# Kernel tuning notes

Hardware: AMD Instinct MI355X
Metric: run time of the kernel (lower is better)

Reference implementation:

```python
import jax, jax.numpy as jnp
import numpy as np
from jax import lax

B, S, F_IN, H = 64, 512, 128, 512

def setup_inputs() -> dict:
    key = jax.random.key(0)
    ks = jax.random.split(key, 7)
    s = 1.0 / np.sqrt(H)
    return {
        "inputs": jax.random.normal(ks[0], (B, S, F_IN), dtype=jnp.float32),
        "W_ih": jax.random.normal(ks[1], (4 * H, F_IN), dtype=jnp.float32) * s,
        "W_hh": jax.random.normal(ks[2], (4 * H, H), dtype=jnp.float32) * s,
        "b_ih": jax.random.normal(ks[3], (4 * H,), dtype=jnp.float32) * s,
        "b_hh": jax.random.normal(ks[4], (4 * H,), dtype=jnp.float32) * s,
        "W_out": jax.random.normal(ks[5], (F_IN, H), dtype=jnp.float32) * s,
        "b_out": jax.random.normal(ks[6], (F_IN,), dtype=jnp.float32) * s,
    }

def reference(inputs, W_ih, W_hh, b_ih, b_hh, W_out, b_out):
    # inputs: [B, S, F]. Inference path: y=None, future=0 -> scan over all S steps.
    b, seq, _ = inputs.shape
    h = W_hh.shape[1]
    # Precompute input-to-gate projections for all timesteps: [S, B, 4H]
    x_gates = jnp.einsum("bsf,gf->sbg", inputs, W_ih) + b_ih + b_hh

    def step(carry, xg):
        h_t, c_t = carry
        gates = xg + h_t @ W_hh.T  # [B, 4H]
        i_g, f_g, g_g, o_g = jnp.split(gates, 4, axis=-1)
        i_g = jax.nn.sigmoid(i_g)
        f_g = jax.nn.sigmoid(f_g)
        g_g = jnp.tanh(g_g)
        o_g = jax.nn.sigmoid(o_g)
        c_t = f_g * c_t + i_g * g_g
        h_t = o_g * jnp.tanh(c_t)
        out = h_t @ W_out.T + b_out  # [B, F]
        return (h_t, c_t), out

    h0 = jnp.zeros((b, h), dtype=inputs.dtype)
    c0 = jnp.zeros((b, h), dtype=inputs.dtype)
    _, outs = lax.scan(step, (h0, c0), x_gates)  # outs: [S, B, F]
    return jnp.transpose(outs, (1, 0, 2))  # [B, S, F]
```

## Files before the change

kernel.cpp:

```cpp
#include <hip/hip_runtime.h>

typedef float f32x4 __attribute__((ext_vector_type(4)));

namespace {
constexpr int Bn = 64, Sn = 512, Fn = 128, Hn = 512;
constexpr int NWG = 256, NTHR = 512;
constexpr int HXS = 644;
constexpr int PQS = 581;
constexpr int RING0 = 1024;
}

__device__ __forceinline__ float sigmoid_f(float v) {
    return 1.0f / (1.0f + __expf(-v));
}
__device__ __forceinline__ float tanh_f(float v) {
    v = fminf(fmaxf(v, -15.0f), 15.0f);
    const float e = __expf(-2.0f * v);
    return (1.0f - e) / (1.0f + e);
}

__global__ __launch_bounds__(NTHR, 2)
void lstm_persist(const float* __restrict__ x,
                  const float* __restrict__ Wih,
                  const float* __restrict__ Whh,
                  const float* __restrict__ bih,
                  const float* __restrict__ bhh,
                  const float* __restrict__ Wout,
                  const float* __restrict__ bout,
                  float* __restrict__ out,
                  float* __restrict__ ws)
{
    const int w = blockIdx.x, t = threadIdx.x;
    const int bw = w & 7, rw = w >> 3;

    const int q  = t & 31;
    const int r4 = t >> 5;
    const int k0 = 20 * q;

    const int out_fi  = (t >> 1) & 3;
    const int out_bb  = (t >> 3) & 7;
    const int out_ksl = ((t >> 6) << 1) | (t & 1);

    __shared__ float hx[8][HXS];
    __shared__ float part[32 * PQS];
    __shared__ float opart[4][8][9];
    __shared__ float gb[64];
    __shared__ float cst[16][9];
    __shared__ float bo[4];

    f32x4 wreg[4][5];
#pragma unroll
    for (int i = 0; i < 4; ++i) {
        const int r = 4 * r4 + i;
        const int G = (r >> 4) * Hn + rw * 16 + (r & 15);
#pragma unroll
        for (int j = 0; j < 5; ++j) {
            const int kk = k0 + 4 * j;
            if (kk < Hn) wreg[i][j] = *(const f32x4*)(Whh + (size_t)G * Hn + kk);
            else         wreg[i][j] = *(const f32x4*)(Wih + (size_t)G * Fn + (kk - Hn));
        }
    }

    if (t < 64) {
        const int G = (t >> 4) * Hn + rw * 16 + (t & 15);
        gb[t] = bih[G] + bhh[G];
    }
    if (t < 4) bo[t] = bout[rw * 4 + t];
    if (t < 128) cst[t >> 3][t & 7] = 0.0f;

    unsigned* const bar = (unsigned*)ws;
    float* const ring = ws + RING0;

    if (t < 128) {
        const int ul = t & 15, bb = (t >> 4) & 7;
        float* hdst = ring + (size_t)(Bn * Hn) +
                      (size_t)(8 * bw + bb) * Hn + (16 * rw + ul);
        const float z = 0.0f;
        asm volatile("global_store_dword %0, %1, off sc0 sc1"
                     :: "v"(hdst), "v"(z) : "memory");
    }
    asm volatile("s_waitcnt vmcnt(0)" ::: "memory");
    __syncthreads();
    if (t == 0) {
        unsigned* gcnt = bar + 32 * ((w >> 4) + 1);
        const unsigned old = atomicAdd(gcnt, 1u);
        if (old == 15u) atomicAdd(bar, 1u);
        int guard = 0;
        while (__hip_atomic_load(bar, __ATOMIC_RELAXED,
                                 __HIP_MEMORY_SCOPE_AGENT) < 16u) {
            __builtin_amdgcn_s_sleep(1);
            if (++guard > 100000) break;
        }
    }
    __syncthreads();

    for (int k = 0; k <= Sn; ++k) {
        const int slot = (k & 1) ^ 1;
        const float* hsrc = ring + (size_t)slot * (Bn * Hn) + (size_t)bw * 8 * Hn;
        f32x4 v0, v1;
        {
            const float* p0 = hsrc + 4 * t;
            const float* p1 = p0 + 2048;
            asm volatile(
                "global_load_dwordx4 %0, %2, off sc0 sc1\n\t"
                "global_load_dwordx4 %1, %3, off sc0 sc1\n\t"
                "s_waitcnt vmcnt(0)"
                : "=&v"(v0), "=&v"(v1)
                : "v"(p0), "v"(p1));
        }
        {
            int fi = t;
            *(f32x4*)&hx[fi >> 7][(fi & 127) * 4] = v0;
            fi = t + 512;
            *(f32x4*)&hx[fi >> 7][(fi & 127) * 4] = v1;
        }
        if (k < Sn && t < 256) {
            const int bb = t >> 5, f4 = (t & 31) * 4;
            const f32x4 v = *(const f32x4*)(x + (size_t)(8 * bw + bb) * Sn * Fn +
                                            (size_t)k * Fn + f4);
            *(f32x4*)&hx[bb][Hn + f4] = v;
        }
        __syncthreads();

        if (k < Sn) {
            float acc[4][8];
#pragma unroll
            for (int i = 0; i < 4; ++i)
#pragma unroll
                for (int ib = 0; ib < 8; ++ib) acc[i][ib] = 0.0f;
#pragma unroll
            for (int j = 0; j < 5; ++j) {
                f32x4 hv[4];
#pragma unroll
                for (int ib = 0; ib < 4; ++ib)
                    hv[ib] = *(const f32x4*)&hx[ib][k0 + 4 * j];
#pragma unroll
                for (int i = 0; i < 4; ++i)
#pragma unroll
                    for (int ib = 0; ib < 4; ++ib)
                        acc[i][ib] += wreg[i][j].x * hv[ib].x + wreg[i][j].y * hv[ib].y +
                                      wreg[i][j].z * hv[ib].z + wreg[i][j].w * hv[ib].w;
#pragma unroll
                for (int ib = 0; ib < 4; ++ib)
                    hv[ib] = *(const f32x4*)&hx[4 + ib][k0 + 4 * j];
#pragma unroll
                for (int i = 0; i < 4; ++i)
#pragma unroll
                    for (int ib = 0; ib < 4; ++ib)
                        acc[i][4 + ib] += wreg[i][j].x * hv[ib].x + wreg[i][j].y * hv[ib].y +
                                          wreg[i][j].z * hv[ib].z + wreg[i][j].w * hv[ib].w;
            }
#pragma unroll
            for (int i = 0; i < 4; ++i)
#pragma unroll
                for (int ib = 0; ib < 8; ++ib)
                    part[q * PQS + (4 * r4 + i) * 9 + ib] = acc[i][ib];
        }

        if (k >= 1 && t < 256) {
            const float* wo = Wout + (size_t)(rw * 4 + out_fi) * Hn + out_ksl * 64;
            const float* hrow = &hx[out_bb][out_ksl * 64];
            float oa = 0.0f;
#pragma unroll
            for (int jj = 0; jj < 16; ++jj) {
                const f32x4 wv = *(const f32x4*)(wo + 4 * jj);
                const f32x4 hv = *(const f32x4*)(hrow + 4 * jj);
                oa += wv.x * hv.x + wv.y * hv.y + wv.z * hv.z + wv.w * hv.w;
            }
            opart[out_fi][out_bb][out_ksl] = oa;
        }
        __syncthreads();

        if (k < Sn && t < 128) {
            const int ul = t & 15, bb = (t >> 4) & 7;
            float g4[4];
#pragma unroll
            for (int gate = 0; gate < 4; ++gate) {
                const int r = gate * 16 + ul;
                float s = gb[r];
#pragma unroll
                for (int qq = 0; qq < 32; ++qq) s += part[qq * PQS + r * 9 + bb];
                g4[gate] = s;
            }
            const float ig = sigmoid_f(g4[0]);
            const float fg = sigmoid_f(g4[1]);
            const float gg = tanh_f(g4[2]);
            const float og = sigmoid_f(g4[3]);
            const float cn = fg * cst[ul][bb] + ig * gg;
            cst[ul][bb] = cn;
            const float hn = og * tanh_f(cn);
            float* hdst = ring + (size_t)(k & 1) * (Bn * Hn) +
                          (size_t)(8 * bw + bb) * Hn + (16 * rw + ul);
            asm volatile("global_store_dword %0, %1, off sc0 sc1"
                         :: "v"(hdst), "v"(hn) : "memory");
        } else if (k >= 1 && t >= 128 && t < 160) {
            const int fi = (t - 128) >> 3, bb = (t - 128) & 7;
            float s = bo[fi];
#pragma unroll
            for (int qq = 0; qq < 8; ++qq) s += opart[fi][bb][qq];
            out[(size_t)(8 * bw + bb) * Sn * Fn + (size_t)(k - 1) * Fn + rw * 4 + fi] = s;
        }

        if (k < Sn) {
            asm volatile("s_waitcnt vmcnt(0)" ::: "memory");
            __syncthreads();
            if (t == 0) {
                const unsigned gen = (unsigned)(k + 2);
                unsigned* gcnt = bar + 32 * ((w >> 4) + 1);
                const unsigned old = atomicAdd(gcnt, 1u);
                if (old == 16u * gen - 1u) atomicAdd(bar, 1u);
                const unsigned target = 16u * gen;
                int guard = 0;
                while (__hip_atomic_load(bar, __ATOMIC_RELAXED,
                                         __HIP_MEMORY_SCOPE_AGENT) < target) {
                    __builtin_amdgcn_s_sleep(1);
                    if (++guard > 100000) break;
                }
            }
            __syncthreads();
        }
    }
}

extern "C" void kernel_launch(void* const* d_in, const int* in_sizes, int n_in,
                              void* d_out, int out_size, void* d_ws, size_t ws_size,
                              hipStream_t stream) {
    (void)in_sizes; (void)n_in; (void)out_size; (void)ws_size;
    const float* x    = (const float*)d_in[0];
    const float* Wih  = (const float*)d_in[1];
    const float* Whh  = (const float*)d_in[2];
    const float* bih  = (const float*)d_in[3];
    const float* bhh  = (const float*)d_in[4];
    const float* Wout = (const float*)d_in[5];
    const float* bout = (const float*)d_in[6];
    float* out = (float*)d_out;
    float* wsp = (float*)d_ws;

    hipMemsetAsync(d_ws, 0, 4096, stream);

    lstm_persist<<<dim3(NWG), dim3(NTHR), 0, stream>>>(
        x, Wih, Whh, bih, bhh, Wout, bout, out, wsp);
}
```

Measured before the change: 8.990 ms.

## Group workgroups by XCC and use per-XCC barriers with local h rings

Each workgroup reads its XCC id from a hardware register and claims a slot with an atomic, so the batch group is mapped to one XCC and all h exchange stays among workgroups on the same die. The two-level global barrier becomes a per-group counter polled by every thread, and loads and stores drop the sc1 bit on the assumption that the data stays in that XCC's L2. Workgroups double to 1024 threads, which splits the batch dimension of the recurrent matvec and the output projection across more threads and adds a shuffle-based gate split. The scheme relies on exactly 32 workgroups landing on each XCC and on the barrier counter region not being cleared by the 4096-byte memset beyond its range, so a different scheduler placement could deadlock or give wrong results.

```diff
diff --git a/kernel.cpp b/kernel.cpp
--- a/kernel.cpp
+++ b/kernel.cpp
@@ -4,10 +4,11 @@
 
 namespace {
 constexpr int Bn = 64, Sn = 512, Fn = 128, Hn = 512;
-constexpr int NWG = 256, NTHR = 512;
+constexpr int NWG = 256, NTHR = 1024;
 constexpr int HXS = 644;
 constexpr int PQS = 581;
 constexpr int RING0 = 1024;
+constexpr int GRP_RING = 8192;
 }
 
 __device__ __forceinline__ float sigmoid_f(float v) {
@@ -19,7 +20,7 @@
     return (1.0f - e) / (1.0f + e);
 }
 
-__global__ __launch_bounds__(NTHR, 2)
+__global__ __launch_bounds__(NTHR)
 void lstm_persist(const float* __restrict__ x,
                   const float* __restrict__ Wih,
                   const float* __restrict__ Whh,
@@ -30,11 +31,26 @@
                   float* __restrict__ out,
                   float* __restrict__ ws)
 {
-    const int w = blockIdx.x, t = threadIdx.x;
-    const int bw = w & 7, rw = w >> 3;
+    const int t = threadIdx.x;
+
+    __shared__ int s_grp[2];
+    if (t == 0) {
+        const unsigned xcc =
+            (unsigned)__builtin_amdgcn_s_getreg(20 | (0 << 6) | (3 << 11)) & 7u;
+        unsigned* slotp = (unsigned*)ws + 256 + 32 * xcc;
+        s_grp[0] = (int)xcc;
+        s_grp[1] = (int)(atomicAdd(slotp, 1u) & 31u);
+    }
+    __syncthreads();
+    const int bw = s_grp[0];
+    const int rw = s_grp[1];
+
+    unsigned* const gcnt = (unsigned*)ws + 32 * bw;
+    float* const ring = ws + RING0 + (size_t)bw * GRP_RING;
 
     const int q  = t & 31;
-    const int r4 = t >> 5;
+    const int r4 = (t >> 5) & 15;
+    const int bh = t >> 9;
     const int k0 = 20 * q;
 
     const int out_fi  = (t >> 1) & 3;
@@ -43,7 +59,7 @@
 
     __shared__ float hx[8][HXS];
     __shared__ float part[32 * PQS];
-    __shared__ float opart[4][8][9];
+    __shared__ float opart[4][8][17];
     __shared__ float gb[64];
     __shared__ float cst[16][9];
     __shared__ float bo[4];
@@ -68,101 +84,75 @@
     if (t < 4) bo[t] = bout[rw * 4 + t];
     if (t < 128) cst[t >> 3][t & 7] = 0.0f;
 
-    unsigned* const bar = (unsigned*)ws;
-    float* const ring = ws + RING0;
-
     if (t < 128) {
-        const int ul = t & 15, bb = (t >> 4) & 7;
-        float* hdst = ring + (size_t)(Bn * Hn) +
-                      (size_t)(8 * bw + bb) * Hn + (16 * rw + ul);
+        const int ul = t & 15, bbc = (t >> 4) & 7;
+        float* hdst = ring + 4096 + (size_t)bbc * 512 + (16 * rw + ul);
         const float z = 0.0f;
-        asm volatile("global_store_dword %0, %1, off sc0 sc1"
+        asm volatile("global_store_dword %0, %1, off sc0"
                      :: "v"(hdst), "v"(z) : "memory");
     }
     asm volatile("s_waitcnt vmcnt(0)" ::: "memory");
     __syncthreads();
-    if (t == 0) {
-        unsigned* gcnt = bar + 32 * ((w >> 4) + 1);
-        const unsigned old = atomicAdd(gcnt, 1u);
-        if (old == 15u) atomicAdd(bar, 1u);
+    if (t == 0) atomicAdd(gcnt, 1u);
+    {
         int guard = 0;
-        while (__hip_atomic_load(bar, __ATOMIC_RELAXED,
-                                 __HIP_MEMORY_SCOPE_AGENT) < 16u) {
+        while (__hip_atomic_load(gcnt, __ATOMIC_RELAXED,
+                                 __HIP_MEMORY_SCOPE_AGENT) < 32u) {
             __builtin_amdgcn_s_sleep(1);
-            if (++guard > 100000) break;
-        }
-    }
-    __syncthreads();
+            if (++guard > 1000000) break;
+        }
+    }
 
     for (int k = 0; k <= Sn; ++k) {
         const int slot = (k & 1) ^ 1;
-        const float* hsrc = ring + (size_t)slot * (Bn * Hn) + (size_t)bw * 8 * Hn;
-        f32x4 v0, v1;
         {
-            const float* p0 = hsrc + 4 * t;
-            const float* p1 = p0 + 2048;
-            asm volatile(
-                "global_load_dwordx4 %0, %2, off sc0 sc1\n\t"
-                "global_load_dwordx4 %1, %3, off sc0 sc1\n\t"
-                "s_waitcnt vmcnt(0)"
-                : "=&v"(v0), "=&v"(v1)
-                : "v"(p0), "v"(p1));
-        }
-        {
-            int fi = t;
-            *(f32x4*)&hx[fi >> 7][(fi & 127) * 4] = v0;
-            fi = t + 512;
-            *(f32x4*)&hx[fi >> 7][(fi & 127) * 4] = v1;
+            const float* p0 = ring + (size_t)slot * 4096 + 4 * t;
+            f32x4 v0;
+            asm volatile("global_load_dwordx4 %0, %1, off sc0\n\t"
+                         "s_waitcnt vmcnt(0)"
+                         : "=&v"(v0) : "v"(p0) : "memory");
+            *(f32x4*)&hx[t >> 7][(t & 127) * 4] = v0;
         }
         if (k < Sn && t < 256) {
-            const int bb = t >> 5, f4 = (t & 31) * 4;
-            const f32x4 v = *(const f32x4*)(x + (size_t)(8 * bw + bb) * Sn * Fn +
+            const int bbs = t >> 5, f4 = (t & 31) * 4;
+            const f32x4 v = *(const f32x4*)(x + (size_t)(8 * bw + bbs) * Sn * Fn +
                                             (size_t)k * Fn + f4);
-            *(f32x4*)&hx[bb][Hn + f4] = v;
+            *(f32x4*)&hx[bbs][Hn + f4] = v;
         }
         __syncthreads();
 
         if (k < Sn) {
-            float acc[4][8];
+            float acc[4][4];
 #pragma unroll
             for (int i = 0; i < 4; ++i)
 #pragma unroll
-                for (int ib = 0; ib < 8; ++ib) acc[i][ib] = 0.0f;
+                for (int ib = 0; ib < 4; ++ib) acc[i][ib] = 0.0f;
 #pragma unroll
             for (int j = 0; j < 5; ++j) {
                 f32x4 hv[4];
 #pragma unroll
                 for (int ib = 0; ib < 4; ++ib)
-                    hv[ib] = *(const f32x4*)&hx[ib][k0 + 4 * j];
+                    hv[ib] = *(const f32x4*)&hx[4 * bh + ib][k0 + 4 * j];
 #pragma unroll
                 for (int i = 0; i < 4; ++i)
 #pragma unroll
                     for (int ib = 0; ib < 4; ++ib)
                         acc[i][ib] += wreg[i][j].x * hv[ib].x + wreg[i][j].y * hv[ib].y +
                                       wreg[i][j].z * hv[ib].z + wreg[i][j].w * hv[ib].w;
+            }
+#pragma unroll
+            for (int i = 0; i < 4; ++i)
 #pragma unroll
                 for (int ib = 0; ib < 4; ++ib)
-                    hv[ib] = *(const f32x4*)&hx[4 + ib][k0 + 4 * j];
-#pragma unroll
-                for (int i = 0; i < 4; ++i)
-#pragma unroll
-                    for (int ib = 0; ib < 4; ++ib)
-                        acc[i][4 + ib] += wreg[i][j].x * hv[ib].x + wreg[i][j].y * hv[ib].y +
-                                          wreg[i][j].z * hv[ib].z + wreg[i][j].w * hv[ib].w;
-            }
-#pragma unroll
-            for (int i = 0; i < 4; ++i)
-#pragma unroll
-                for (int ib = 0; ib < 8; ++ib)
-                    part[q * PQS + (4 * r4 + i) * 9 + ib] = acc[i][ib];
-        }
-
-        if (k >= 1 && t < 256) {
-            const float* wo = Wout + (size_t)(rw * 4 + out_fi) * Hn + out_ksl * 64;
-            const float* hrow = &hx[out_bb][out_ksl * 64];
+                    part[q * PQS + (4 * r4 + i) * 9 + (4 * bh + ib)] = acc[i][ib];
+        }
+
+        if (k >= 1 && t < 512) {
+            const float* wo = Wout + (size_t)(rw * 4 + out_fi) * Hn + out_ksl * 32;
+            const float* hrow = &hx[out_bb][out_ksl * 32];
             float oa = 0.0f;
 #pragma unroll
-            for (int jj = 0; jj < 16; ++jj) {
+            for (int jj = 0; jj < 8; ++jj) {
                 const f32x4 wv = *(const f32x4*)(wo + 4 * jj);
                 const f32x4 hv = *(const f32x4*)(hrow + 4 * jj);
                 oa += wv.x * hv.x + wv.y * hv.y + wv.z * hv.z + wv.w * hv.w;
@@ -171,53 +161,50 @@
         }
         __syncthreads();
 
-        if (k < Sn && t < 128) {
-            const int ul = t & 15, bb = (t >> 4) & 7;
-            float g4[4];
-#pragma unroll
-            for (int gate = 0; gate < 4; ++gate) {
-                const int r = gate * 16 + ul;
-                float s = gb[r];
-#pragma unroll
-                for (int qq = 0; qq < 32; ++qq) s += part[qq * PQS + r * 9 + bb];
-                g4[gate] = s;
-            }
-            const float ig = sigmoid_f(g4[0]);
-            const float fg = sigmoid_f(g4[1]);
-            const float gg = tanh_f(g4[2]);
-            const float og = sigmoid_f(g4[3]);
-            const float cn = fg * cst[ul][bb] + ig * gg;
-            cst[ul][bb] = cn;
-            const float hn = og * tanh_f(cn);
-            float* hdst = ring + (size_t)(k & 1) * (Bn * Hn) +
-                          (size_t)(8 * bw + bb) * Hn + (16 * rw + ul);
-            asm volatile("global_store_dword %0, %1, off sc0 sc1"
-                         :: "v"(hdst), "v"(hn) : "memory");
-        } else if (k >= 1 && t >= 128 && t < 160) {
-            const int fi = (t - 128) >> 3, bb = (t - 128) & 7;
+        if (k < Sn && t < 256) {
+            const int gh = t & 1, ul = (t >> 1) & 15, bbc = (t >> 5) & 7;
+            const int r0 = (2 * gh) * 16 + ul, r1 = (2 * gh + 1) * 16 + ul;
+            float s0 = gb[r0], s1 = gb[r1];
+#pragma unroll
+            for (int qq = 0; qq < 32; ++qq) {
+                s0 += part[qq * PQS + r0 * 9 + bbc];
+                s1 += part[qq * PQS + r1 * 9 + bbc];
+            }
+            const float o0 = __shfl_xor(s0, 1, 64);
+            const float o1 = __shfl_xor(s1, 1, 64);
+            if (gh == 0) {
+                const float ig = sigmoid_f(s0);
+                const float fg = sigmoid_f(s1);
+                const float gg = tanh_f(o0);
+                const float og = sigmoid_f(o1);
+                const float cn = fg * cst[ul][bbc] + ig * gg;
+                cst[ul][bbc] = cn;
+                const float hn = og * tanh_f(cn);
+                float* hdst = ring + (size_t)(k & 1) * 4096 +
+                              (size_t)bbc * 512 + (16 * rw + ul);
+                asm volatile("global_store_dword %0, %1, off sc0"
+                             :: "v"(hdst), "v"(hn) : "memory");
+            }
+        } else if (k >= 1 && t >= 256 && t < 288) {
+            const int fi = (t - 256) >> 3, bbo = (t - 256) & 7;
             float s = bo[fi];
 #pragma unroll
-            for (int qq = 0; qq < 8; ++qq) s += opart[fi][bb][qq];
-            out[(size_t)(8 * bw + bb) * Sn * Fn + (size_t)(k - 1) * Fn + rw * 4 + fi] = s;
+            for (int qq = 0; qq < 16; ++qq) s += opart[fi][bbo][qq];
+            out[(size_t)(8 * bw + bbo) * Sn * Fn + (size_t)(k - 1) * Fn +
+                rw * 4 + fi] = s;
         }
 
         if (k < Sn) {
             asm volatile("s_waitcnt vmcnt(0)" ::: "memory");
             __syncthreads();
-            if (t == 0) {
-                const unsigned gen = (unsigned)(k + 2);
-                unsigned* gcnt = bar + 32 * ((w >> 4) + 1);
-                const unsigned old = atomicAdd(gcnt, 1u);
-                if (old == 16u * gen - 1u) atomicAdd(bar, 1u);
-                const unsigned target = 16u * gen;
-                int guard = 0;
-                while (__hip_atomic_load(bar, __ATOMIC_RELAXED,
-                                         __HIP_MEMORY_SCOPE_AGENT) < target) {
-                    __builtin_amdgcn_s_sleep(1);
-                    if (++guard > 100000) break;
-                }
-            }
-            __syncthreads();
+            if (t == 0) atomicAdd(gcnt, 1u);
+            const unsigned target = 32u * (unsigned)(k + 2);
+            int guard = 0;
+            while (__hip_atomic_load(gcnt, __ATOMIC_RELAXED,
+                                     __HIP_MEMORY_SCOPE_AGENT) < target) {
+                __builtin_amdgcn_s_sleep(1);
+                if (++guard > 100000) break;
+            }
         }
     }
 }
@@ -233,11 +220,11 @@
     const float* bhh  = (const float*)d_in[4];
     const float* Wout = (const float*)d_in[5];
     const float* bout = (const float*)d_in[6];
-    float* out = (float*)d_out;
-    float* wsp = (float*)d_ws;
+    float* outp = (float*)d_out;
+    float* wsp  = (float*)d_ws;
 
     hipMemsetAsync(d_ws, 0, 4096, stream);
 
     lstm_persist<<<dim3(NWG), dim3(NTHR), 0, stream>>>(
-        x, Wih, Whh, bih, bhh, Wout, bout, out, wsp);
-}
+        x, Wih, Whh, bih, bhh, Wout, bout, outp, wsp);
+}
```

Measured after the change: 13.64 ms. 51.7% more time.
